# Kernel optimization log

Hardware: AMD Instinct MI355X
Metric: run time of the kernel (lower is better)

Reference implementation:

```python
import jax, jax.numpy as jnp
import numpy as np

B, S, D = 2, 2048, 2048
H, DH = 16, 128          # n_heads, head_dim
HFF = 8192               # hidden_dim (SwiGLU)
EPS = 1e-5               # layer_norm_eps passed to AdvancedRMSNorm


def setup_inputs() -> dict:
    key = jax.random.key(0)
    ks = jax.random.split(key, 16)
    sd = lambda fan_in: 1.0 / np.sqrt(fan_in)
    inp = {
        "x": jax.random.normal(ks[0], (B, S, D), jnp.float32),
        # attention (torch Linear weights: [out, in])
        "q_w": jax.random.normal(ks[1], (D, D), jnp.float32) * sd(D),
        "k_w": jax.random.normal(ks[2], (D, D), jnp.float32) * sd(D),
        "v_w": jax.random.normal(ks[3], (D, D), jnp.float32) * sd(D),
        "o_w": jax.random.normal(ks[4], (D, D), jnp.float32) * sd(D),
        "temp": jnp.ones((H, 1, 1), jnp.float32),  # learnable per-head temperature
        # RMSNorm scales
        "ln1_w": jnp.ones((D,), jnp.float32),
        "ln2_w": jnp.ones((D,), jnp.float32),
        # SwiGLU
        "gate_w": jax.random.normal(ks[5], (HFF, D), jnp.float32) * sd(D),
        "up_w": jax.random.normal(ks[6], (HFF, D), jnp.float32) * sd(D),
        "gate2_w": jax.random.normal(ks[7], (HFF, D), jnp.float32) * sd(D),
        "down_w": jax.random.normal(ks[8], (D, HFF), jnp.float32) * sd(HFF),
        # gated residual connections (Linear with bias)
        "ag_w": jax.random.normal(ks[9], (D, D), jnp.float32) * sd(D),
        "ag_b": jnp.zeros((D,), jnp.float32),
        "fg_w": jax.random.normal(ks[10], (D, D), jnp.float32) * sd(D),
        "fg_b": jnp.zeros((D,), jnp.float32),
    }
    return inp


def _rmsnorm(x, w):
    rms = jnp.sqrt(jnp.mean(x * x, axis=-1, keepdims=True) + EPS)
    return w * (x / rms)


def _l2norm(x):
    # F.normalize(dim=-1): x / max(||x||_2, 1e-12)
    n = jnp.sqrt(jnp.sum(x * x, axis=-1, keepdims=True))
    return x / jnp.maximum(n, 1e-12)


def _block(x, q_w, k_w, v_w, o_w, temp, ln1_w, ln2_w,
           gate_w, up_w, gate2_w, down_w, ag_w, ag_b, fg_w, fg_b):
    # --- cosine-sim attention sublayer ---
    residual = x
    h = _rmsnorm(x, ln1_w)
    q = (h @ q_w.T).reshape(B, S, H, DH).transpose(0, 2, 1, 3)  # [B,H,S,DH]
    k = (h @ k_w.T).reshape(B, S, H, DH).transpose(0, 2, 1, 3)
    v = (h @ v_w.T).reshape(B, S, H, DH).transpose(0, 2, 1, 3)
    q = _l2norm(q)
    k = _l2norm(k)
    scores = jnp.einsum("bhqd,bhkd->bhqk", q, k) * temp  # temp [H,1,1] broadcasts
    causal = jnp.triu(jnp.ones((S, S), bool), k=1)
    scores = jnp.where(causal, -jnp.inf, scores)
    attn = jax.nn.softmax(scores, axis=-1)
    out = jnp.einsum("bhqk,bhkd->bhqd", attn, v)
    out = out.transpose(0, 2, 1, 3).reshape(B, S, D)
    attn_out = out @ o_w.T
    # gated residual: sigmoid(W a + b)*a + (1-g)*residual
    g = jax.nn.sigmoid(attn_out @ ag_w.T + ag_b)
    x = g * attn_out + (1.0 - g) * residual
    # --- SwiGLU sublayer ---
    residual = x
    h = _rmsnorm(x, ln2_w)
    gate = jax.nn.silu(h @ gate_w.T)
    up = h @ up_w.T
    gate2 = jax.nn.sigmoid(h @ gate2_w.T)
    ffn_out = (gate * up * gate2) @ down_w.T
    g = jax.nn.sigmoid(ffn_out @ fg_w.T + fg_b)
    return g * ffn_out + (1.0 - g) * residual


def reference(x, q_w, k_w, v_w, o_w, temp, ln1_w, ln2_w,
              gate_w, up_w, gate2_w, down_w, ag_w, ag_b, fg_w, fg_b):
    return _block(x, q_w, k_w, v_w, o_w, temp, ln1_w, ln2_w,
                  gate_w, up_w, gate2_w, down_w, ag_w, ag_b, fg_w, fg_b)
```

## Files before the change

kernel.cpp:

```cpp
#include <hip/hip_runtime.h>

typedef unsigned short u16;
typedef unsigned int u32;
using bf16x8 = __attribute__((ext_vector_type(8))) short;
using f32x4  = __attribute__((ext_vector_type(4))) float;

#define EPS 1e-5f

__device__ __forceinline__ u16 f2bf(float f) {
    union { float f; u32 u; } v; v.f = f;
    u32 r = v.u + 0x7FFFu + ((v.u >> 16) & 1u);
    return (u16)(r >> 16);
}
__device__ __forceinline__ float bf2f(u16 u) {
    union { u32 u; float f; } v; v.u = ((u32)u) << 16;
    return v.f;
}
__device__ __forceinline__ void gl16(const void* g, void* s) {
    __builtin_amdgcn_global_load_lds(
        (const __attribute__((address_space(1))) u32*)g,
        (__attribute__((address_space(3))) u32*)s, 16, 0, 0);
}
__device__ __forceinline__ float sigm(float x) { return 1.f / (1.f + __expf(-x)); }

__global__ void conv_bf16(const float* __restrict__ src, u16* __restrict__ dst, int n4) {
    int i = blockIdx.x * 256 + threadIdx.x;
    if (i >= n4) return;
    float4 v = reinterpret_cast<const float4*>(src)[i];
    u32 lo = (u32)f2bf(v.x) | ((u32)f2bf(v.y) << 16);
    u32 hi = (u32)f2bf(v.z) | ((u32)f2bf(v.w) << 16);
    reinterpret_cast<uint2*>(dst)[i] = make_uint2(lo, hi);
}

__global__ void conv3_bf16(const float* __restrict__ s0, const float* __restrict__ s1,
                           const float* __restrict__ s2, u16* __restrict__ d0,
                           u16* __restrict__ d1, u16* __restrict__ d2, int n4) {
    int i = blockIdx.x * 256 + threadIdx.x;
    if (i >= n4) return;
    const float* src = (blockIdx.y == 0) ? s0 : (blockIdx.y == 1) ? s1 : s2;
    u16* dst = (blockIdx.y == 0) ? d0 : (blockIdx.y == 1) ? d1 : d2;
    float4 v = reinterpret_cast<const float4*>(src)[i];
    u32 lo = (u32)f2bf(v.x) | ((u32)f2bf(v.y) << 16);
    u32 hi = (u32)f2bf(v.z) | ((u32)f2bf(v.w) << 16);
    reinterpret_cast<uint2*>(dst)[i] = make_uint2(lo, hi);
}

__global__ void rmsnorm_k(const float* __restrict__ x, const float* __restrict__ wt,
                          u16* __restrict__ out) {
    __shared__ float red[4];
    const int row = blockIdx.x, t = threadIdx.x;
    const float* xr = x + (size_t)row * 2048;
    float4 v0 = *reinterpret_cast<const float4*>(&xr[t * 8]);
    float4 v1 = *reinterpret_cast<const float4*>(&xr[t * 8 + 4]);
    float ss = v0.x*v0.x + v0.y*v0.y + v0.z*v0.z + v0.w*v0.w
             + v1.x*v1.x + v1.y*v1.y + v1.z*v1.z + v1.w*v1.w;
#pragma unroll
    for (int d = 1; d < 64; d <<= 1) ss += __shfl_xor(ss, d);
    if ((t & 63) == 0) red[t >> 6] = ss;
    __syncthreads();
    const float tot = red[0] + red[1] + red[2] + red[3];
    const float s = 1.f / sqrtf(tot * (1.f / 2048.f) + EPS);
    float4 w0 = *reinterpret_cast<const float4*>(&wt[t * 8]);
    float4 w1 = *reinterpret_cast<const float4*>(&wt[t * 8 + 4]);
    u32 o[4];
    o[0] = (u32)f2bf(v0.x * s * w0.x) | ((u32)f2bf(v0.y * s * w0.y) << 16);
    o[1] = (u32)f2bf(v0.z * s * w0.z) | ((u32)f2bf(v0.w * s * w0.w) << 16);
    o[2] = (u32)f2bf(v1.x * s * w1.x) | ((u32)f2bf(v1.y * s * w1.y) << 16);
    o[3] = (u32)f2bf(v1.z * s * w1.z) | ((u32)f2bf(v1.w * s * w1.w) << 16);
    *reinterpret_cast<uint4*>(&out[(size_t)row * 2048 + t * 8]) =
        make_uint4(o[0], o[1], o[2], o[3]);
}

__global__ void qk_l2norm(u16* __restrict__ qkv, const float* __restrict__ temp) {
    const int wid = blockIdx.x * 4 + (threadIdx.x >> 6);
    const int l = threadIdx.x & 63;
    const int n = wid >> 5;
    const int rem = wid & 31;
    const int which = rem >> 4;
    const int h = rem & 15;
    u16* p = qkv + (size_t)n * 6144 + which * 2048 + h * 128 + l * 2;
    u32 v = *reinterpret_cast<const u32*>(p);
    float f0 = bf2f((u16)(v & 0xffff)), f1 = bf2f((u16)(v >> 16));
    float ss = f0 * f0 + f1 * f1;
#pragma unroll
    for (int d = 1; d < 64; d <<= 1) ss += __shfl_xor(ss, d);
    float sc = 1.f / fmaxf(sqrtf(ss), 1e-12f);
    if (which == 0) sc *= temp[h];
    *reinterpret_cast<u32*>(p) = (u32)f2bf(f0 * sc) | ((u32)f2bf(f1 * sc) << 16);
}

template <int EPI>
__global__ __launch_bounds__(512, 1)
void gemm_u(const u16* __restrict__ A, const u16* __restrict__ B,
            float* __restrict__ outF, u16* __restrict__ outB,
            const float* __restrict__ bias, const float* __restrict__ addend,
            const float* __restrict__ resid, float* __restrict__ outG,
            int M, int N, int K, int ldc) {
    extern __shared__ u16 lds[];
    const int nbn = N >> 8;
    const int nwg = (M >> 7) * nbn;
    const int orig = blockIdx.x;
    const int q8 = nwg >> 3, r8 = nwg & 7;
    const int xcd = orig & 7, lin = orig >> 3;
    const int wgid = (xcd < r8 ? xcd * (q8 + 1) : r8 * (q8 + 1) + (xcd - r8) * q8) + lin;
    const int g = wgid / (nbn << 3);
    const int rem = wgid - g * (nbn << 3);
    const int bn = rem >> 3;
    const int bm = (g << 3) + (rem & 7);

    const int t = threadIdx.x;
    const int w = t >> 6, l = t & 63;
    const int wr = w >> 2, wc = w & 3;
    const int lr = l & 15, lg = l >> 4;
    const int NT = K >> 6;

    const int pr = t >> 3, ps = t & 7;
    const int sg = ps ^ (pr & 7);
    const u16* aSrc = A + (size_t)(bm * 128 + pr) * K + sg * 8;
    const u16* bSrc = B + (size_t)(bn * 256 + pr) * K + sg * 8;
    const size_t rowStep = (size_t)64 * K;

#define STG_A(bi, ko) do { u16* da = lds + (bi) * 24576 + t * 8;                 \
        gl16(aSrc + (ko), da); gl16(aSrc + rowStep + (ko), da + 4096); } while (0)
#define STG_B01(bi, ko) do { u16* db = lds + (bi) * 24576 + 8192 + t * 8;        \
        gl16(bSrc + (ko), db); gl16(bSrc + rowStep + (ko), db + 4096); } while (0)
#define STG_B23(bi, ko) do { u16* db = lds + (bi) * 24576 + 8192 + t * 8;        \
        gl16(bSrc + 2 * rowStep + (ko), db + 8192);                              \
        gl16(bSrc + 3 * rowStep + (ko), db + 12288); } while (0)

    f32x4 acc[4][4];
#pragma unroll
    for (int i = 0; i < 4; i++)
#pragma unroll
        for (int j = 0; j < 4; j++) acc[i][j] = (f32x4){0.f, 0.f, 0.f, 0.f};

    const int xr = (lr & 7) << 4;
    const int kof[2] = { ((lg) << 4) ^ xr, ((4 + lg) << 4) ^ xr };

    STG_A(0, 0); STG_B01(0, 0); STG_B23(0, 0);
    asm volatile("s_waitcnt vmcnt(0)" ::: "memory");
    __builtin_amdgcn_s_barrier();

    for (int T = 0; T < NT; ++T) {
        const char* bufA = (const char*)lds + (size_t)(T & 1) * 49152;
        const char* bufB = bufA + 16384;
        const int sbi = (T + 1) & 1;
        const bool st = (T + 1) < NT;
        const size_t ko = (size_t)(T + 1) * 64;
        bf16x8 bf[4][2];
#pragma unroll
        for (int n = 0; n < 4; n++) {
            const int rb = wc * 64 + n * 16 + lr;
            bf[n][0] = *reinterpret_cast<const bf16x8*>(bufB + rb * 128 + kof[0]);
            bf[n][1] = *reinterpret_cast<const bf16x8*>(bufB + rb * 128 + kof[1]);
        }
#pragma unroll
        for (int p = 0; p < 4; ++p) {
            const int ks = p >> 1, mh = p & 1;
            bf16x8 af[2];
#pragma unroll
            for (int m2 = 0; m2 < 2; m2++) {
                const int ra = wr * 64 + (mh * 2 + m2) * 16 + lr;
                af[m2] = *reinterpret_cast<const bf16x8*>(bufA + ra * 128 + kof[ks]);
            }
            if (st) {
                if (p == 0) STG_A(sbi, ko);
                if (p == 1) STG_B01(sbi, ko);
                if (p == 2) STG_B23(sbi, ko);
            }
            __builtin_amdgcn_s_setprio(1);
#pragma unroll
            for (int m2 = 0; m2 < 2; m2++)
#pragma unroll
                for (int n = 0; n < 4; n++)
                    acc[mh * 2 + m2][n] = __builtin_amdgcn_mfma_f32_16x16x32_bf16(
                        af[m2], bf[n][ks], acc[mh * 2 + m2][n], 0, 0, 0);
            __builtin_amdgcn_s_setprio(0);
        }
        if (st) {
            asm volatile("s_waitcnt vmcnt(0)" ::: "memory");
            __builtin_amdgcn_s_barrier();
        }
    }
#undef STG_A
#undef STG_B01
#undef STG_B23

#pragma unroll
    for (int m = 0; m < 4; m++) {
        const int row = bm * 128 + wr * 64 + m * 16 + lg * 4;
#pragma unroll
        for (int n = 0; n < 4; n++) {
            const int col = bn * 256 + wc * 64 + n * 16 + lr;
#pragma unroll
            for (int q = 0; q < 4; q++) {
                const size_t idx = (size_t)(row + q) * ldc + col;
                const float v = acc[m][n][q];
                if (EPI == 0) {
                    outB[idx] = f2bf(v);
                } else if (EPI == 1) {
                    outF[idx] = v;
                    outB[idx] = f2bf(v);
                } else {
                    const float g2 = sigm(v + bias[col]);
                    outG[idx] = g2 * addend[idx] + (1.f - g2) * resid[idx];
                }
            }
        }
    }
}

#define VSWZ(dh) (((((dh) >> 3) ^ (dh)) & 7) << 4)
__global__ __launch_bounds__(512) void flash_attn(const u16* __restrict__ qkv,
                                                  u16* __restrict__ out) {
    __shared__ u16 klds[2][64 * 128];
    __shared__ u16 vlds[2][128 * 64];
    __shared__ u16 plds[8][16 * 64];
    const int t = threadIdx.x, w = t >> 6, l = t & 63;
    const int lr = l & 15, lg = l >> 4;
    const int b0 = blockIdx.x;
    const int xcd = b0 & 7, i0 = b0 >> 3;
    const int bh = ((i0 & 3) << 3) | xcd;
    const int p = i0 >> 2;
    const int b = bh >> 4, h = bh & 15;
    const size_t base = (size_t)b * 2048;
    const int sr0 = t >> 4;
    const int sc0 = (t & 15) << 3;

    uint4 kreg0, kreg1, vreg0, vreg1;

#define STAGE_LOAD(KT) do {                                                          \
        const size_t gg = (base + (size_t)(KT) * 64 + sr0) * 6144 + h * 128 + sc0;   \
        kreg0 = *reinterpret_cast<const uint4*>(&qkv[gg + 2048]);                    \
        vreg0 = *reinterpret_cast<const uint4*>(&qkv[gg + 4096]);                    \
        kreg1 = *reinterpret_cast<const uint4*>(&qkv[gg + 32 * 6144 + 2048]);        \
        vreg1 = *reinterpret_cast<const uint4*>(&qkv[gg + 32 * 6144 + 4096]);        \
    } while (0)

#define STAGE_WRITE(BUF) do {                                                                     \
        char* kb = (char*)&klds[BUF][0];                                                          \
        char* vb = (char*)&vlds[BUF][0];                                                          \
        *reinterpret_cast<uint4*>(kb + ((sr0 * 256 + sc0 * 2) ^ ((sr0 & 7) << 4))) = kreg0;       \
        *reinterpret_cast<uint4*>(kb + (((sr0 + 32) * 256 + sc0 * 2) ^ ((sr0 & 7) << 4))) = kreg1;\
        union { uint4 u; u16 s[8]; } vv;                                                          \
        vv.u = vreg0;                                                                             \
        _Pragma("unroll")                                                                         \
        for (int jj = 0; jj < 8; jj++) {                                                          \
            const int dh = sc0 + jj;                                                              \
            *reinterpret_cast<u16*>(vb + ((dh * 128 + sr0 * 2) ^ VSWZ(dh))) = vv.s[jj];           \
        }                                                                                         \
        vv.u = vreg1;                                                                             \
        _Pragma("unroll")                                                                         \
        for (int jj = 0; jj < 8; jj++) {                                                          \
            const int dh = sc0 + jj;                                                              \
            *reinterpret_cast<u16*>(vb + ((dh * 128 + (sr0 + 32) * 2) ^ VSWZ(dh))) = vv.s[jj];    \
        }                                                                                         \
    } while (0)

    for (int phase = 0; phase < 2; ++phase) {
        const int qt = phase ? (15 - p) : p;
        const int last = 2 * qt + 1;
        const int qrow = qt * 128 + w * 16 + lr;
        const int qr0 = qt * 128 + w * 16 + lg * 4;
        bf16x8 qf[4];
#pragma unroll
        for (int kk = 0; kk < 4; kk++)
            qf[kk] = *reinterpret_cast<const bf16x8*>(
                &qkv[(base + qrow) * 6144 + h * 128 + kk * 32 + lg * 8]);
        f32x4 o[8];
#pragma unroll
        for (int i = 0; i < 8; i++) o[i] = (f32x4){0.f, 0.f, 0.f, 0.f};
        float m[4] = {-1e30f, -1e30f, -1e30f, -1e30f};
        float ls[4] = {0.f, 0.f, 0.f, 0.f};

        STAGE_LOAD(0);
        int cur = 0;
        STAGE_WRITE(0);
        __syncthreads();

        for (int kt = 0; kt <= last; ++kt) {
            if (kt < last) STAGE_LOAD(kt + 1);
            const char* kb = (const char*)&klds[cur][0];
            const char* vb = (const char*)&vlds[cur][0];
            f32x4 s[4];
#pragma unroll
            for (int nf = 0; nf < 4; nf++) {
                f32x4 a = (f32x4){0.f, 0.f, 0.f, 0.f};
                const int kv = nf * 16 + lr;
#pragma unroll
                for (int kk = 0; kk < 4; kk++) {
                    bf16x8 kf = *reinterpret_cast<const bf16x8*>(
                        kb + ((kv * 256 + kk * 64 + lg * 16) ^ ((kv & 7) << 4)));
                    a = __builtin_amdgcn_mfma_f32_16x16x32_bf16(qf[kk], kf, a, 0, 0, 0);
                }
                s[nf] = a;
            }
            if (kt >= 2 * qt) {
#pragma unroll
                for (int nf = 0; nf < 4; nf++) {
                    const int kvi = kt * 64 + nf * 16 + lr;
#pragma unroll
                    for (int q = 0; q < 4; q++)
                        if (kvi > qr0 + q) s[nf][q] = -1e30f;
                }
            }
            float mx[4] = {-1e30f, -1e30f, -1e30f, -1e30f};
#pragma unroll
            for (int nf = 0; nf < 4; nf++)
#pragma unroll
                for (int q = 0; q < 4; q++) mx[q] = fmaxf(mx[q], s[nf][q]);
#pragma unroll
            for (int q = 0; q < 4; q++) {
#pragma unroll
                for (int d = 1; d < 16; d <<= 1) mx[q] = fmaxf(mx[q], __shfl_xor(mx[q], d));
            }
            float fac[4], rs[4];
#pragma unroll
            for (int q = 0; q < 4; q++) {
                const float mn = fmaxf(m[q], mx[q]);
                fac[q] = __expf(m[q] - mn);
                m[q] = mn;
                rs[q] = 0.f;
            }
#pragma unroll
            for (int nf = 0; nf < 4; nf++) {
#pragma unroll
                for (int q = 0; q < 4; q++) {
                    const float pv = __expf(s[nf][q] - m[q]);
                    s[nf][q] = pv;
                    rs[q] += pv;
                }
            }
#pragma unroll
            for (int nf = 0; nf < 4; nf++) {
                const int col = nf * 16 + lr;
#pragma unroll
                for (int q = 0; q < 4; q++) {
                    const int row = lg * 4 + q;
                    *reinterpret_cast<u16*>((char*)&plds[w][0] +
                        ((row * 128 + col * 2) ^ ((row & 7) << 4))) = f2bf(s[nf][q]);
                }
            }
#pragma unroll
            for (int q = 0; q < 4; q++) {
#pragma unroll
                for (int d = 1; d < 16; d <<= 1) rs[q] += __shfl_xor(rs[q], d);
                ls[q] = ls[q] * fac[q] + rs[q];
            }
#pragma unroll
            for (int nf2 = 0; nf2 < 8; nf2++)
#pragma unroll
                for (int q = 0; q < 4; q++) o[nf2][q] *= fac[q];
#pragma unroll
            for (int ks = 0; ks < 2; ks++) {
                bf16x8 pf = *reinterpret_cast<const bf16x8*>((char*)&plds[w][0] +
                    ((lr * 128 + ks * 64 + lg * 16) ^ ((lr & 7) << 4)));
#pragma unroll
                for (int nf2 = 0; nf2 < 8; nf2++) {
                    const int dh = nf2 * 16 + lr;
                    bf16x8 vf = *reinterpret_cast<const bf16x8*>(
                        vb + ((dh * 128 + ks * 64 + lg * 16) ^ VSWZ(dh)));
                    o[nf2] = __builtin_amdgcn_mfma_f32_16x16x32_bf16(pf, vf, o[nf2], 0, 0, 0);
                }
            }
            if (kt < last) STAGE_WRITE(cur ^ 1);
            __syncthreads();
            cur ^= 1;
        }
#pragma unroll
        for (int nf2 = 0; nf2 < 8; nf2++) {
            const int col = h * 128 + nf2 * 16 + lr;
#pragma unroll
            for (int q = 0; q < 4; q++) {
                const float v = o[nf2][q] / ls[q];
                out[(base + qr0 + q) * 2048 + col] = f2bf(v);
            }
        }
        __syncthreads();
    }
#undef STAGE_LOAD
#undef STAGE_WRITE
}

__global__ void swiglu_comb(const u16* __restrict__ f3, u16* __restrict__ comb) {
    const size_t u = (size_t)blockIdx.x * 256 + threadIdx.x;
    const size_t n = u >> 8;
    const int f = (int)(u & 255) << 3;
    const u16* gp = f3 + n * 6144 + f;
    union { uint4 q; u16 s[8]; } g, up, g2;
    g.q  = *reinterpret_cast<const uint4*>(gp);
    up.q = *reinterpret_cast<const uint4*>(gp + 2048);
    g2.q = *reinterpret_cast<const uint4*>(gp + 4096);
    u32 r[4];
#pragma unroll
    for (int i = 0; i < 4; i++) {
        float a0 = bf2f(g.s[2 * i]),     a1 = bf2f(g.s[2 * i + 1]);
        float b0 = bf2f(up.s[2 * i]),    b1 = bf2f(up.s[2 * i + 1]);
        float c0 = bf2f(g2.s[2 * i]),    c1 = bf2f(g2.s[2 * i + 1]);
        float r0 = a0 * sigm(a0) * b0 * sigm(c0);
        float r1 = a1 * sigm(a1) * b1 * sigm(c1);
        r[i] = (u32)f2bf(r0) | ((u32)f2bf(r1) << 16);
    }
    *reinterpret_cast<uint4*>(comb + n * 8192 + f) = make_uint4(r[0], r[1], r[2], r[3]);
}

extern "C" void kernel_launch(void* const* d_in, const int* in_sizes, int n_in,
                              void* d_out, int out_size, void* d_ws, size_t ws_size,
                              hipStream_t stream) {
    const float* x      = (const float*)d_in[0];
    const float* q_w    = (const float*)d_in[1];
    const float* k_w    = (const float*)d_in[2];
    const float* v_w    = (const float*)d_in[3];
    const float* o_w    = (const float*)d_in[4];
    const float* temp   = (const float*)d_in[5];
    const float* ln1_w  = (const float*)d_in[6];
    const float* ln2_w  = (const float*)d_in[7];
    const float* gate_w = (const float*)d_in[8];
    const float* up_w   = (const float*)d_in[9];
    const float* gate2_w= (const float*)d_in[10];
    const float* down_w = (const float*)d_in[11];
    const float* ag_w   = (const float*)d_in[12];
    const float* ag_b   = (const float*)d_in[13];
    const float* fg_w   = (const float*)d_in[14];
    const float* fg_b   = (const float*)d_in[15];

    const int GEMM_LDS = 98304;
    (void)hipFuncSetAttribute(reinterpret_cast<const void*>(&gemm_u<0>),
                              hipFuncAttributeMaxDynamicSharedMemorySize, GEMM_LDS);
    (void)hipFuncSetAttribute(reinterpret_cast<const void*>(&gemm_u<1>),
                              hipFuncAttributeMaxDynamicSharedMemorySize, GEMM_LDS);
    (void)hipFuncSetAttribute(reinterpret_cast<const void*>(&gemm_u<2>),
                              hipFuncAttributeMaxDynamicSharedMemorySize, GEMM_LDS);

    char* ws = (char*)d_ws;
    u16*  Wbuf = (u16*)(ws);
    u16*  hbuf = (u16*)(ws + 33554432);
    float* x1  = (float*)(ws + 50331648);
    u16*  combo= (u16*)(ws + 83886080);
    char* E    = ws + 150994944;
    char* F    = ws + 201326592;
    u16*  ffb  = (u16*)(ws + 234881024);

    u16*   qkvact = (u16*)E;
    float* aof    = (float*)E;
    u16*   aob    = (u16*)(E + 33554432);
    u16*   ffn3q  = (u16*)E;
    u16*   attnb  = (u16*)F;
    float* fff    = (float*)F;

    float* outp = (float*)d_out;
    const size_t DD = 2048ull * 2048ull;
    const int cg_d = (int)(DD / 4) / 256;
    const int GRID_BIG = 32 * 24;
    const int GRID_SM  = 32 * 8;

    hipLaunchKernelGGL(rmsnorm_k, dim3(4096), dim3(256), 0, stream, x, ln1_w, hbuf);

    hipLaunchKernelGGL(conv3_bf16, dim3(cg_d, 3), dim3(256), 0, stream,
                       q_w, k_w, v_w, Wbuf, Wbuf + DD, Wbuf + 2 * DD, (int)(DD / 4));
    hipLaunchKernelGGL((gemm_u<0>), dim3(GRID_BIG), dim3(512), GEMM_LDS, stream,
                       hbuf, Wbuf, (float*)nullptr, qkvact,
                       (const float*)nullptr, (const float*)nullptr, (const float*)nullptr,
                       (float*)nullptr, 4096, 6144, 2048, 6144);

    hipLaunchKernelGGL(qk_l2norm, dim3(32768), dim3(256), 0, stream, qkvact, temp);

    hipLaunchKernelGGL(flash_attn, dim3(256), dim3(512), 0, stream, qkvact, attnb);

    hipLaunchKernelGGL(conv_bf16, dim3(cg_d), dim3(256), 0, stream, o_w, Wbuf, (int)(DD / 4));
    hipLaunchKernelGGL((gemm_u<1>), dim3(GRID_SM), dim3(512), GEMM_LDS, stream,
                       attnb, Wbuf, aof, aob,
                       (const float*)nullptr, (const float*)nullptr, (const float*)nullptr,
                       (float*)nullptr, 4096, 2048, 2048, 2048);

    hipLaunchKernelGGL(conv_bf16, dim3(cg_d), dim3(256), 0, stream, ag_w, Wbuf, (int)(DD / 4));
    hipLaunchKernelGGL((gemm_u<2>), dim3(GRID_SM), dim3(512), GEMM_LDS, stream,
                       aob, Wbuf, (float*)nullptr, (u16*)nullptr,
                       ag_b, aof, x, x1, 4096, 2048, 2048, 2048);

    hipLaunchKernelGGL(rmsnorm_k, dim3(4096), dim3(256), 0, stream, x1, ln2_w, hbuf);

    for (int qd = 0; qd < 4; qd++) {
        const size_t wofs = (size_t)qd * 2048 * 2048;
        hipLaunchKernelGGL(conv3_bf16, dim3(cg_d, 3), dim3(256), 0, stream,
                           gate_w + wofs, up_w + wofs, gate2_w + wofs,
                           Wbuf, Wbuf + 2048 * 2048, Wbuf + 2ull * 2048 * 2048, (int)(DD / 4));
        hipLaunchKernelGGL((gemm_u<0>), dim3(GRID_BIG), dim3(512), GEMM_LDS, stream,
                           hbuf, Wbuf, (float*)nullptr, ffn3q,
                           (const float*)nullptr, (const float*)nullptr, (const float*)nullptr,
                           (float*)nullptr, 4096, 6144, 2048, 6144);
        hipLaunchKernelGGL(swiglu_comb, dim3(4096), dim3(256), 0, stream, ffn3q, combo + qd * 2048);
    }

    hipLaunchKernelGGL(conv_bf16, dim3(16384), dim3(256), 0, stream, down_w, Wbuf, (int)(2048ull * 8192 / 4));
    hipLaunchKernelGGL((gemm_u<1>), dim3(GRID_SM), dim3(512), GEMM_LDS, stream,
                       combo, Wbuf, fff, ffb,
                       (const float*)nullptr, (const float*)nullptr, (const float*)nullptr,
                       (float*)nullptr, 4096, 2048, 8192, 2048);

    hipLaunchKernelGGL(conv_bf16, dim3(cg_d), dim3(256), 0, stream, fg_w, Wbuf, (int)(DD / 4));
    hipLaunchKernelGGL((gemm_u<2>), dim3(GRID_SM), dim3(512), GEMM_LDS, stream,
                       ffb, Wbuf, (float*)nullptr, (u16*)nullptr,
                       fg_b, fff, x1, outp, 4096, 2048, 2048, 2048);
}
```

Before: 1.098 ms.

## Add 256x256-tile bf16 GEMM for the wide QKV and SwiGLU projections

Adds a new GEMM kernel that uses 256x256 output tiles with double-buffered LDS staging (128 KB), replacing the 128x256 tile kernel for the five N=6144 projection GEMMs. Each workgroup now holds an 8x4 grid of MFMA accumulators per wave, which raises arithmetic intensity and cuts global and LDS traffic per flop. The grid halves to 384 workgroups on 256 CUs, so the final wave is only half full, and register pressure from the larger accumulator set could limit scheduling.

```diff
diff --git a/kernel.cpp b/kernel.cpp
--- a/kernel.cpp
+++ b/kernel.cpp
@@ -87,6 +87,121 @@
     float sc = 1.f / fmaxf(sqrtf(ss), 1e-12f);
     if (which == 0) sc *= temp[h];
     *reinterpret_cast<u32*>(p) = (u32)f2bf(f0 * sc) | ((u32)f2bf(f1 * sc) << 16);
+}
+
+__global__ __launch_bounds__(512, 1)
+void gemm_big8(const u16* __restrict__ A, const u16* __restrict__ B,
+               u16* __restrict__ outB, int M, int N, int K, int ldc) {
+    extern __shared__ u16 lds[];
+    const int nbn = N >> 8;
+    const int nwg = (M >> 8) * nbn;
+    const int orig = blockIdx.x;
+    const int q8 = nwg >> 3, r8 = nwg & 7;
+    const int xcd = orig & 7, lin = orig >> 3;
+    const int wgid = (xcd < r8 ? xcd * (q8 + 1) : r8 * (q8 + 1) + (xcd - r8) * q8) + lin;
+    const int g = wgid / (nbn << 2);
+    const int rem = wgid - g * (nbn << 2);
+    const int bn = rem >> 2;
+    const int bm = (g << 2) + (rem & 3);
+
+    const int t = threadIdx.x;
+    const int w = t >> 6, l = t & 63;
+    const int wr = w >> 2, wc = w & 3;
+    const int lr = l & 15, lg = l >> 4;
+    const int NT = K >> 6;
+
+    const int srow = t >> 3;
+    const int scg  = (t & 7) ^ (srow & 7);
+    const u16* aS0 = A + (size_t)(bm * 256 + srow) * K + scg * 8;
+    const u16* aS1 = aS0 + (size_t)128 * K;
+    const u16* bS0 = B + (size_t)(bn * 256 + srow) * K + scg * 8;
+    const u16* bS1 = bS0 + (size_t)128 * K;
+    const size_t r64 = (size_t)64 * K;
+
+#define STG(slot, src, ko) do {                                     \
+        gl16((src) + (ko), (slot) + t * 8);                         \
+        gl16((src) + (ko) + r64, (slot) + 4096 + t * 8);            \
+    } while (0)
+#define STG_TILE(bi, ko) do {                                       \
+        u16* bb = lds + (bi) * 32768;                               \
+        STG(bb + 16384, bS0, ko);                                   \
+        STG(bb + 24576, bS1, ko);                                   \
+        STG(bb + 0,     aS0, ko);                                   \
+        STG(bb + 8192,  aS1, ko);                                   \
+    } while (0)
+
+    f32x4 acc[8][4];
+#pragma unroll
+    for (int i = 0; i < 8; i++)
+#pragma unroll
+        for (int j = 0; j < 4; j++) acc[i][j] = (f32x4){0.f, 0.f, 0.f, 0.f};
+
+    const int xr = (lr & 7) << 4;
+    const int kof[2] = { ((lg) << 4) ^ xr, ((4 + lg) << 4) ^ xr };
+
+    STG_TILE(0, 0);
+    asm volatile("s_waitcnt vmcnt(2)" ::: "memory");
+    __builtin_amdgcn_s_barrier();
+
+    for (int T = 0; T < NT; ++T) {
+        const char* base = (const char*)lds + (size_t)(T & 1) * 65536;
+        const int sbi = (T + 1) & 1;
+        const bool st = (T + 1) < NT;
+        const size_t ko = (size_t)(T + 1) * 64;
+        const char* aB = base + wr * 16384;
+        const char* bB = base + 32768 + (wc >> 1) * 16384 + (wc & 1) * 8192;
+        bf16x8 bfr[4][2];
+
+#pragma unroll
+        for (int p = 0; p < 4; ++p) {
+            const int ks = p >> 1, mh = p & 1;
+            bf16x8 af[4];
+#pragma unroll
+            for (int m2 = 0; m2 < 4; m2++) {
+                const int ra = mh * 64 + m2 * 16 + lr;
+                af[m2] = *reinterpret_cast<const bf16x8*>(aB + ra * 128 + kof[ks]);
+            }
+            if (p == 0) {
+#pragma unroll
+                for (int n = 0; n < 4; n++) {
+                    const int rb = n * 16 + lr;
+                    bfr[n][0] = *reinterpret_cast<const bf16x8*>(bB + rb * 128 + kof[0]);
+                    bfr[n][1] = *reinterpret_cast<const bf16x8*>(bB + rb * 128 + kof[1]);
+                }
+                if (st) STG_TILE(sbi, ko);
+            }
+            __builtin_amdgcn_s_barrier();
+            __builtin_amdgcn_s_setprio(1);
+#pragma unroll
+            for (int m2 = 0; m2 < 4; m2++)
+#pragma unroll
+                for (int n = 0; n < 4; n++)
+                    acc[mh * 4 + m2][n] = __builtin_amdgcn_mfma_f32_16x16x32_bf16(
+                        af[m2], bfr[n][ks], acc[mh * 4 + m2][n], 0, 0, 0);
+            __builtin_amdgcn_s_setprio(0);
+            if (p == 0) {
+                if (st) asm volatile("s_waitcnt vmcnt(8)" ::: "memory");
+                else    asm volatile("s_waitcnt vmcnt(0)" ::: "memory");
+            }
+            if (p == 3 && st)
+                asm volatile("s_waitcnt vmcnt(2)" ::: "memory");
+            __builtin_amdgcn_s_barrier();
+        }
+    }
+#undef STG
+#undef STG_TILE
+
+#pragma unroll
+    for (int m = 0; m < 8; m++) {
+        const int row = bm * 256 + wr * 128 + m * 16 + lg * 4;
+#pragma unroll
+        for (int n = 0; n < 4; n++) {
+            const int col = bn * 256 + wc * 64 + n * 16 + lr;
+#pragma unroll
+            for (int q = 0; q < 4; q++)
+                outB[(size_t)(row + q) * ldc + col] = f2bf(acc[m][n][q]);
+        }
+    }
 }
 
 template <int EPI>
@@ -425,12 +540,15 @@
     const float* fg_b   = (const float*)d_in[15];
 
     const int GEMM_LDS = 98304;
+    const int BIG_LDS  = 131072;
     (void)hipFuncSetAttribute(reinterpret_cast<const void*>(&gemm_u<0>),
                               hipFuncAttributeMaxDynamicSharedMemorySize, GEMM_LDS);
     (void)hipFuncSetAttribute(reinterpret_cast<const void*>(&gemm_u<1>),
                               hipFuncAttributeMaxDynamicSharedMemorySize, GEMM_LDS);
     (void)hipFuncSetAttribute(reinterpret_cast<const void*>(&gemm_u<2>),
                               hipFuncAttributeMaxDynamicSharedMemorySize, GEMM_LDS);
+    (void)hipFuncSetAttribute(reinterpret_cast<const void*>(&gemm_big8),
+                              hipFuncAttributeMaxDynamicSharedMemorySize, BIG_LDS);
 
     char* ws = (char*)d_ws;
     u16*  Wbuf = (u16*)(ws);
@@ -451,17 +569,15 @@
     float* outp = (float*)d_out;
     const size_t DD = 2048ull * 2048ull;
     const int cg_d = (int)(DD / 4) / 256;
-    const int GRID_BIG = 32 * 24;
+    const int GRID_BIG = 16 * 24;
     const int GRID_SM  = 32 * 8;
 
     hipLaunchKernelGGL(rmsnorm_k, dim3(4096), dim3(256), 0, stream, x, ln1_w, hbuf);
 
     hipLaunchKernelGGL(conv3_bf16, dim3(cg_d, 3), dim3(256), 0, stream,
                        q_w, k_w, v_w, Wbuf, Wbuf + DD, Wbuf + 2 * DD, (int)(DD / 4));
-    hipLaunchKernelGGL((gemm_u<0>), dim3(GRID_BIG), dim3(512), GEMM_LDS, stream,
-                       hbuf, Wbuf, (float*)nullptr, qkvact,
-                       (const float*)nullptr, (const float*)nullptr, (const float*)nullptr,
-                       (float*)nullptr, 4096, 6144, 2048, 6144);
+    hipLaunchKernelGGL(gemm_big8, dim3(GRID_BIG), dim3(512), BIG_LDS, stream,
+                       hbuf, Wbuf, qkvact, 4096, 6144, 2048, 6144);
 
     hipLaunchKernelGGL(qk_l2norm, dim3(32768), dim3(256), 0, stream, qkvact, temp);
 
@@ -485,10 +601,8 @@
         hipLaunchKernelGGL(conv3_bf16, dim3(cg_d, 3), dim3(256), 0, stream,
                            gate_w + wofs, up_w + wofs, gate2_w + wofs,
                            Wbuf, Wbuf + 2048 * 2048, Wbuf + 2ull * 2048 * 2048, (int)(DD / 4));
-        hipLaunchKernelGGL((gemm_u<0>), dim3(GRID_BIG), dim3(512), GEMM_LDS, stream,
-                           hbuf, Wbuf, (float*)nullptr, ffn3q,
-                           (const float*)nullptr, (const float*)nullptr, (const float*)nullptr,
-                           (float*)nullptr, 4096, 6144, 2048, 6144);
+        hipLaunchKernelGGL(gemm_big8, dim3(GRID_BIG), dim3(512), BIG_LDS, stream,
+                           hbuf, Wbuf, ffn3q, 4096, 6144, 2048, 6144);
         hipLaunchKernelGGL(swiglu_comb, dim3(4096), dim3(256), 0, stream, ffn3q, combo + qd * 2048);
     }
 
```

After: 1.182 ms. 1.08x slower.
